# Kernel tuning notes

Measured on AMD Instinct MI355X. Metric: run time of the kernel, lower is better.

Reference implementation:

```python
import jax, jax.numpy as jnp
import numpy as np
from jax import lax

B, S, D, H = 2, 2048, 1024, 16
DH = D // H
KERNELS = (3, 5)
NK = len(KERNELS)
COUT = D // NK  # channels per conv branch


def setup_inputs() -> dict:
    key = jax.random.key(0)
    ks = jax.random.split(key, 12)
    w = lambda k, shp: (jax.random.normal(k, shp, dtype=jnp.float32) * 0.02)
    inp = {
        "q": jax.random.normal(ks[0], (B, S, D), dtype=jnp.float32),
        "k": jax.random.normal(ks[1], (B, S, D), dtype=jnp.float32),
        "v": jax.random.normal(ks[2], (B, S, D), dtype=jnp.float32),
        "mask": jnp.ones((B, S, S), dtype=jnp.int32),
        "Wq": w(ks[3], (D, D)),
        "Wk": w(ks[4], (D, D)),
        "Wv": w(ks[5], (D, D)),
        "Wo": w(ks[6], (D, D)),
        "bo": jnp.zeros((D,), dtype=jnp.float32),
        "conv_w0": w(ks[7], (COUT, D, KERNELS[0])),  # OIH
        "conv_b0": jnp.zeros((COUT,), dtype=jnp.float32),
        "conv_w1": w(ks[8], (COUT, D, KERNELS[1])),
        "conv_b1": jnp.zeros((COUT,), dtype=jnp.float32),
        "gate": jnp.ones((H,), dtype=jnp.float32),
    }
    return inp


def _split_heads(x):  # [B,S,D] -> [B,H,S,DH]
    return x.reshape(B, S, H, DH).transpose(0, 2, 1, 3)


def _conv1d_same(x_ncl, w_oik, b, ksz):
    pad = ksz // 2
    y = lax.conv_general_dilated(
        x_ncl, w_oik, window_strides=(1,), padding=[(pad, pad)],
        dimension_numbers=("NCH", "OIH", "NCH"))
    return y + b[None, :, None]


def reference(q, k, v, mask, Wq, Wk, Wv, Wo, bo,
              conv_w0, conv_b0, conv_w1, conv_b1, gate):
    qh = _split_heads(q @ Wq.T)
    kh = _split_heads(k @ Wk.T)
    vh = _split_heads(v @ Wv.T)

    # conv-derived K: operate on raw k in NCL layout, concat channel-wise
    k_ncl = k.transpose(0, 2, 1)  # [B,D,S]
    c0 = _conv1d_same(k_ncl, conv_w0, conv_b0, KERNELS[0])
    c1 = _conv1d_same(k_ncl, conv_w1, conv_b1, KERNELS[1])
    k_conv = jnp.concatenate([c0, c1], axis=1).transpose(0, 2, 1)  # [B,S,D]
    kch = _split_heads(k_conv)

    g = jax.nn.sigmoid(gate).reshape(1, H, 1, 1)
    scale = 1.0 / np.sqrt(DH).astype(np.float32)
    attn = ((1.0 - g) * jnp.einsum("bhqd,bhkd->bhqk", qh, kh)
            + g * jnp.einsum("bhqd,bhkd->bhqk", qh, kch)) * scale
    attn = jnp.where(mask[:, None, :, :] == 0, jnp.float32(-1e9), attn)
    attn = jax.nn.softmax(attn, axis=-1)

    out = jnp.einsum("bhqk,bhkd->bhqd", attn, vh)  # [B,H,S,DH]
    out = out.transpose(0, 2, 1, 3).reshape(B, S, D)
    return out @ Wo.T + bo
```

## Files before the change

### kernel.cpp

```cpp
#include <hip/hip_runtime.h>
#include <math.h>

#define Bb 2
#define Ss 2048
#define Dd 1024
#define Hh 16
#define SP 2052

typedef unsigned short u16;
typedef __bf16 bf16x8 __attribute__((ext_vector_type(8)));
typedef float f32x4 __attribute__((ext_vector_type(4)));
typedef unsigned short u16x8 __attribute__((ext_vector_type(8)));

__device__ __forceinline__ u16 f2bf(float f) {
    union { float f; unsigned int u; } c; c.f = f;
    unsigned int u = c.u + 0x7FFFu + ((c.u >> 16) & 1u);
    return (u16)(u >> 16);
}

__device__ __forceinline__ u16 f2bfn(float f) {
    __bf16 h = (__bf16)f;
    union { __bf16 h; u16 u; } c; c.h = h;
    return c.u;
}

__device__ __forceinline__ float bf2f(u16 h) {
    union { unsigned int u; float f; } c; c.u = ((unsigned int)h) << 16;
    return c.f;
}

__device__ __forceinline__ void gload16(const void* g, void* l) {
    __builtin_amdgcn_global_load_lds(
        (const __attribute__((address_space(1))) void*)g,
        (__attribute__((address_space(3))) void*)l, 16, 0, 0);
}

__global__ void prep_weights(const float* __restrict__ Wq, const float* __restrict__ Wk,
                             const float* __restrict__ Wv, const float* __restrict__ Wo,
                             const float* __restrict__ w0, const float* __restrict__ b0,
                             const float* __restrict__ w1, const float* __restrict__ b1,
                             const float* __restrict__ gate,
                             u16* __restrict__ wqs, u16* __restrict__ wvb, u16* __restrict__ wob,
                             u16* __restrict__ Wc0, u16* __restrict__ Wc1, float* __restrict__ bc)
{
    int idx = blockIdx.x * 256 + threadIdx.x;
    const int NW = 1024 * 1024;
    if (idx < NW) { wqs[idx] = f2bf(Wq[idx] * 0.18033688011112042f); return; }
    idx -= NW;
    if (idx < NW) { wvb[idx] = f2bf(Wv[idx]); return; }
    idx -= NW;
    if (idx < NW) { wob[idx] = f2bf(Wo[idx]); return; }
    idx -= NW;
    if (idx < 512 * 3072) {
        int c = idx / 3072, rem = idx % 3072, t = rem >> 10, d = rem & 1023;
        float g = 1.f / (1.f + expf(-gate[c >> 6]));
        float v = g * w0[(c * 1024 + d) * 3 + t];
        if (t == 1) v += (1.f - g) * Wk[c * 1024 + d];
        Wc0[idx] = f2bf(v);
        return;
    }
    idx -= 512 * 3072;
    if (idx < 512 * 5120) {
        int c = idx / 5120, rem = idx % 5120, t = rem >> 10, d = rem & 1023;
        int cg = c + 512;
        float g = 1.f / (1.f + expf(-gate[cg >> 6]));
        float v = g * w1[(c * 1024 + d) * 5 + t];
        if (t == 2) v += (1.f - g) * Wk[cg * 1024 + d];
        Wc1[idx] = f2bf(v);
        return;
    }
    idx -= 512 * 5120;
    if (idx < 1024) {
        float g = 1.f / (1.f + expf(-gate[idx >> 6]));
        bc[idx] = g * (idx < 512 ? b0[idx] : b1[idx - 512]);
    }
}

__global__ void convert_inputs(const float* __restrict__ q, const float* __restrict__ k,
                               const float* __restrict__ v,
                               u16* __restrict__ qbf, u16* __restrict__ kbf, u16* __restrict__ vbf)
{
    int idx = blockIdx.x * 256 + threadIdx.x;
    const int per = (Bb * SP * Dd) / 8;
    int which = idx / per;
    if (which >= 3) return;
    int e = (idx - which * per) * 8;
    const float* src = which == 0 ? q : which == 1 ? k : v;
    u16* dst = which == 0 ? qbf : which == 1 ? kbf : vbf;
    int rp = e >> 10, col = e & 1023;
    int b = rp / SP, r = rp - b * SP;
    u16x8 o;
    if (r >= 2 && r < SP - 2) {
        const float* s = &src[((size_t)b * Ss + (r - 2)) * Dd + col];
        float4 lo = *(const float4*)s, hi = *(const float4*)(s + 4);
        o[0] = f2bf(lo.x); o[1] = f2bf(lo.y); o[2] = f2bf(lo.z); o[3] = f2bf(lo.w);
        o[4] = f2bf(hi.x); o[5] = f2bf(hi.y); o[6] = f2bf(hi.z); o[7] = f2bf(hi.w);
    } else {
        #pragma unroll
        for (int j = 0; j < 8; j++) o[j] = 0;
    }
    *(u16x8*)&dst[e] = o;
}

__global__ void mask_prep(const int* __restrict__ mask, unsigned int* __restrict__ bits,
                          int* __restrict__ rowflags)
{
    int row = blockIdx.x;
    int lane = threadIdx.x;
    const int* mp = mask + (size_t)row * Ss + lane * 32;
    unsigned int w = 0;
    #pragma unroll
    for (int j = 0; j < 32; j += 4) {
        int4 m4 = *(const int4*)&mp[j];
        if (m4.x != 0) w |= 1u << j;
        if (m4.y != 0) w |= 1u << (j + 1);
        if (m4.z != 0) w |= 1u << (j + 2);
        if (m4.w != 0) w |= 1u << (j + 3);
    }
    bits[(size_t)row * 64 + lane] = w;
    int anyz = __any(w != 0xFFFFFFFFu);
    if (lane == 0) rowflags[row] = anyz;
}

__device__ __forceinline__ void run_gemm_job(
    const u16* __restrict__ A, const u16* __restrict__ B, u16* __restrict__ C,
    int strB, int kS, int kL, int mB, int nB, int rO, int Cst,
    u16* As, u16* Bsh, int lane, int wave, int waveM, int waveN)
{
    f32x4 acc[4][4];
    #pragma unroll
    for (int i = 0; i < 4; i++)
        #pragma unroll
        for (int j = 0; j < 4; j++) acc[i][j] = (f32x4){0.f, 0.f, 0.f, 0.f};

    for (int k0 = kS; k0 < kS + kL; k0 += 32) {
        __syncthreads();
        #pragma unroll
        for (int cc = 0; cc < 2; cc++) {
            int rbase = (wave * 2 + cc) * 16;
            int r = rbase + (lane >> 2);
            int gm = mB + r;
            int grow = (gm >> 11) * SP + (gm & 2047) + rO + (k0 >> 10);
            int csrc = (lane & 3) ^ (r & 3);
            gload16(A + (size_t)grow * 1024 + (k0 & 1023) + csrc * 8, &As[rbase * 32]);
            int gn = nB + r;
            gload16(B + (size_t)gn * strB + k0 + csrc * 8, &Bsh[rbase * 32]);
        }
        __syncthreads();

        bf16x8 af[4], bfr[4];
        #pragma unroll
        for (int t = 0; t < 4; t++) {
            int mrow = waveM + t * 16 + (lane & 15);
            af[t] = *(const bf16x8*)&As[mrow * 32 + (((lane >> 4) ^ (mrow & 3))) * 8];
            int nrow = waveN + t * 16 + (lane & 15);
            bfr[t] = *(const bf16x8*)&Bsh[nrow * 32 + (((lane >> 4) ^ (nrow & 3))) * 8];
        }
        #pragma unroll
        for (int mt = 0; mt < 4; mt++)
            #pragma unroll
            for (int nt = 0; nt < 4; nt++)
                acc[mt][nt] = __builtin_amdgcn_mfma_f32_16x16x32_bf16(
                    af[mt], bfr[nt], acc[mt][nt], 0, 0, 0);
    }

    #pragma unroll
    for (int mt = 0; mt < 4; mt++)
        #pragma unroll
        for (int nt = 0; nt < 4; nt++)
            #pragma unroll
            for (int r = 0; r < 4; r++) {
                int row = mB + waveM + mt * 16 + (lane >> 4) * 4 + r;
                int gcol = nB + waveN + nt * 16 + (lane & 15);
                C[(size_t)row * Cst + gcol] = f2bf(acc[mt][nt][r]);
            }
}

__global__ __launch_bounds__(256) void gemm_multi(
    const u16* __restrict__ qbf, const u16* __restrict__ kbf, const u16* __restrict__ vbf,
    const u16* __restrict__ wqs, const u16* __restrict__ wvb,
    const u16* __restrict__ Wc0, const u16* __restrict__ Wc1,
    u16* __restrict__ Qp, u16* __restrict__ Vp,
    u16* __restrict__ P0a, u16* __restrict__ P0b,
    u16* __restrict__ P1a, u16* __restrict__ P1b, u16* __restrict__ P1c)
{
    __shared__ u16 As[128 * 32];
    __shared__ u16 Bsh[128 * 32];
    int tid = threadIdx.x, lane = tid & 63, wave = tid >> 6;
    int waveM = (wave >> 1) * 64, waveN = (wave & 1) * 64;

    int bid = blockIdx.x;
    const u16 *A0, *B0; u16 *C0; int sB0, kS0, kL0, mB0, nB0, rO0, Cs0;
    const u16 *A1 = nullptr, *B1 = nullptr; u16 *C1 = nullptr;
    int sB1 = 0, kS1 = 0, kL1 = 0, mB1 = 0, nB1 = 0, rO1 = 0, Cs1 = 0;
    int njobs = 1;

    if (bid < 128) {
        int t = bid;
        A0 = kbf; B0 = Wc0; C0 = P0a; sB0 = 3072; kS0 = 0; kL0 = 2048;
        mB0 = (t >> 2) * 128; nB0 = (t & 3) * 128; rO0 = 1; Cs0 = 512;
    } else if (bid < 256) {
        int t = bid - 128;
        A0 = kbf; B0 = Wc1; C0 = P1a; sB0 = 5120; kS0 = 0; kL0 = 2048;
        mB0 = (t >> 2) * 128; nB0 = (t & 3) * 128; rO0 = 0; Cs0 = 512;
    } else if (bid < 384) {
        int t = bid - 256;
        A0 = kbf; B0 = Wc1; C0 = P1b; sB0 = 5120; kS0 = 2048; kL0 = 2048;
        mB0 = (t >> 2) * 128; nB0 = (t & 3) * 128; rO0 = 0; Cs0 = 512;
    } else if (bid < 512) {
        int t = bid - 384;
        A0 = kbf; B0 = Wc0; C0 = P0b; sB0 = 3072; kS0 = 2048; kL0 = 1024;
        mB0 = (t >> 2) * 128; nB0 = (t & 3) * 128; rO0 = 1; Cs0 = 512;
        A1 = kbf; B1 = Wc1; C1 = P1c; sB1 = 5120; kS1 = 4096; kL1 = 1024;
        mB1 = mB0; nB1 = nB0; rO1 = 0; Cs1 = 512;
        njobs = 2;
    } else {
        int i0 = (bid - 512) * 2, i1 = i0 + 1;
        if (i0 < 256) { A0 = qbf; B0 = wqs; C0 = Qp; }
        else { i0 -= 256; A0 = vbf; B0 = wvb; C0 = Vp; }
        sB0 = 1024; kS0 = 0; kL0 = 1024;
        mB0 = (i0 >> 3) * 128; nB0 = (i0 & 7) * 128; rO0 = 2; Cs0 = 1024;
        if (i1 < 256) { A1 = qbf; B1 = wqs; C1 = Qp; }
        else { i1 -= 256; A1 = vbf; B1 = wvb; C1 = Vp; }
        sB1 = 1024; kS1 = 0; kL1 = 1024;
        mB1 = (i1 >> 3) * 128; nB1 = (i1 & 7) * 128; rO1 = 2; Cs1 = 1024;
        njobs = 2;
    }

    run_gemm_job(A0, B0, C0, sB0, kS0, kL0, mB0, nB0, rO0, Cs0,
                 As, Bsh, lane, wave, waveM, waveN);
    if (njobs == 2)
        run_gemm_job(A1, B1, C1, sB1, kS1, kL1, mB1, nB1, rO1, Cs1,
                     As, Bsh, lane, wave, waveM, waveN);
}

__global__ __launch_bounds__(256) void conv_reduce(
    const u16* __restrict__ P0a, const u16* __restrict__ P0b,
    const u16* __restrict__ P1a, const u16* __restrict__ P1b, const u16* __restrict__ P1c,
    const float* __restrict__ bc, u16* __restrict__ Keff)
{
    int idx = blockIdx.x * 256 + threadIdx.x;
    int e = idx * 8;
    int r = e >> 9, c = e & 511;
    u16x8 a0 = *(const u16x8*)&P0a[e];
    u16x8 b0 = *(const u16x8*)&P0b[e];
    u16x8 a1 = *(const u16x8*)&P1a[e];
    u16x8 b1 = *(const u16x8*)&P1b[e];
    u16x8 c1 = *(const u16x8*)&P1c[e];
    float bias0[8], bias1[8];
    *(float4*)&bias0[0] = *(const float4*)&bc[c];
    *(float4*)&bias0[4] = *(const float4*)&bc[c + 4];
    *(float4*)&bias1[0] = *(const float4*)&bc[512 + c];
    *(float4*)&bias1[4] = *(const float4*)&bc[512 + c + 4];
    u16x8 o0, o1;
    #pragma unroll
    for (int j = 0; j < 8; j++) {
        o0[j] = f2bf(bf2f(a0[j]) + bf2f(b0[j]) + bias0[j]);
        o1[j] = f2bf(bf2f(a1[j]) + bf2f(b1[j]) + bf2f(c1[j]) + bias1[j]);
    }
    *(u16x8*)&Keff[(size_t)r * 1024 + c] = o0;
    *(u16x8*)&Keff[(size_t)r * 1024 + 512 + c] = o1;
}

__global__ __launch_bounds__(256) void gemm_out(
    const u16* __restrict__ A, const u16* __restrict__ Bw,
    float* __restrict__ Cf32, const float* __restrict__ bias)
{
    __shared__ u16 As[128 * 32];
    __shared__ u16 Bs[128 * 32];
    int tid = threadIdx.x, lane = tid & 63, wave = tid >> 6;
    int waveM = (wave >> 1) * 64, waveN = (wave & 1) * 64;
    int mBase = blockIdx.y * 128, nBase = blockIdx.x * 128;
    const int K = 1024;

    f32x4 acc[4][4];
    #pragma unroll
    for (int i = 0; i < 4; i++)
        #pragma unroll
        for (int j = 0; j < 4; j++) acc[i][j] = (f32x4){0.f, 0.f, 0.f, 0.f};

    for (int k0 = 0; k0 < K; k0 += 32) {
        __syncthreads();
        #pragma unroll
        for (int cc = 0; cc < 2; cc++) {
            int rbase = (wave * 2 + cc) * 16;
            int r = rbase + (lane >> 2);
            int gm = mBase + r;
            int grow = (gm >> 11) * SP + (gm & 2047) + 2;
            int csrc = (lane & 3) ^ (r & 3);
            gload16(A + (size_t)grow * 1024 + k0 + csrc * 8, &As[rbase * 32]);
            int gn = nBase + r;
            gload16(Bw + (size_t)gn * K + k0 + csrc * 8, &Bs[rbase * 32]);
        }
        __syncthreads();

        bf16x8 af[4], bfr[4];
        #pragma unroll
        for (int t = 0; t < 4; t++) {
            int mrow = waveM + t * 16 + (lane & 15);
            af[t] = *(const bf16x8*)&As[mrow * 32 + (((lane >> 4) ^ (mrow & 3))) * 8];
            int nrow = waveN + t * 16 + (lane & 15);
            bfr[t] = *(const bf16x8*)&Bs[nrow * 32 + (((lane >> 4) ^ (nrow & 3))) * 8];
        }
        #pragma unroll
        for (int mt = 0; mt < 4; mt++)
            #pragma unroll
            for (int nt = 0; nt < 4; nt++)
                acc[mt][nt] = __builtin_amdgcn_mfma_f32_16x16x32_bf16(
                    af[mt], bfr[nt], acc[mt][nt], 0, 0, 0);
    }

    #pragma unroll
    for (int mt = 0; mt < 4; mt++)
        #pragma unroll
        for (int nt = 0; nt < 4; nt++)
            #pragma unroll
            for (int r = 0; r < 4; r++) {
                int row = mBase + waveM + mt * 16 + (lane >> 4) * 4 + r;
                int gcol = nBase + waveN + nt * 16 + (lane & 15);
                Cf32[(size_t)row * 1024 + gcol] = acc[mt][nt][r] + bias[gcol];
            }
}

__global__ __launch_bounds__(256) void vtrans_kernel(const u16* __restrict__ Vp,
                                                     u16* __restrict__ Vt)
{
    __shared__ u16 t[64 * 64];
    int bid = blockIdx.x;
    int st = bid & 31, h = (bid >> 5) & 15, b = bid >> 9;
    int s0 = st * 64;
    int tid = threadIdx.x;
    #pragma unroll
    for (int w = 0; w < 2; w++) {
        int f = tid + w * 256;
        int row = f >> 3, c = f & 7;
        int p = c ^ (row & 7);
        u16x8 v = *(const u16x8*)&Vp[(size_t)(b * Ss + s0 + row) * Dd + h * 64 + c * 8];
        *(u16x8*)&t[row * 64 + p * 8] = v;
    }
    __syncthreads();
    #pragma unroll
    for (int w = 0; w < 2; w++) {
        int f = tid + w * 256;
        int d = f >> 3, s8 = (f & 7) * 8;
        u16x8 v;
        #pragma unroll
        for (int j = 0; j < 8; j++) {
            int s = s8 + j;
            v[j] = t[s * 64 + (((d >> 3) ^ (s & 7))) * 8 + (d & 7)];
        }
        *(u16x8*)&Vt[((size_t)(b * Hh + h) * 64 + d) * Ss + s0 + s8] = v;
    }
}

__global__ __launch_bounds__(256) void flash_kernel(
    const u16* __restrict__ Qp, const u16* __restrict__ Keff, const u16* __restrict__ Vt,
    const unsigned int* __restrict__ maskbits, const int* __restrict__ rowflags,
    u16* __restrict__ AO)
{
    __shared__ u16 Qs[128 * 64];
    __shared__ u16 Ks[64 * 64];
    __shared__ u16 Ps[4][32 * 64];
    int tid = threadIdx.x, lane = tid & 63, wave = tid >> 6;

    int bid = blockIdx.x;
    int xcd = bid & 7, slot = bid >> 3;
    int grp = xcd * 4 + (slot >> 4);
    int q0 = (slot & 15) * 128;
    int h = grp & 15, b = grp >> 4;

    #pragma unroll
    for (int cc = 0; cc < 4; cc++) {
        int rbase = (wave * 4 + cc) * 8;
        int r = rbase + (lane >> 3);
        int csrc = (lane & 7) ^ (r & 7);
        gload16(Qp + (size_t)(b * Ss + q0 + r) * Dd + h * 64 + csrc * 8, &Qs[rbase * 64]);
    }

    int anyz = 0;
    #pragma unroll
    for (int mt = 0; mt < 2; mt++)
        #pragma unroll
        for (int r = 0; r < 4; r++)
            anyz |= rowflags[b * Ss + q0 + wave * 32 + mt * 16 + (lane >> 4) * 4 + r];
    bool doMask = __any(anyz);

    float lrow[2][4];
    f32x4 oa[2][4];
    #pragma unroll
    for (int mt = 0; mt < 2; mt++) {
        #pragma unroll
        for (int r = 0; r < 4; r++) lrow[mt][r] = 0.f;
        #pragma unroll
        for (int nt = 0; nt < 4; nt++) oa[mt][nt] = (f32x4){0.f, 0.f, 0.f, 0.f};
    }

    __syncthreads();

    bf16x8 qa[2][2];
    #pragma unroll
    for (int mt = 0; mt < 2; mt++)
        #pragma unroll
        for (int ks = 0; ks < 2; ks++) {
            int mr = wave * 32 + mt * 16 + (lane & 15);
            int c = ks * 4 + (lane >> 4);
            qa[mt][ks] = *(const bf16x8*)&Qs[mr * 64 + (c ^ (mr & 7)) * 8];
        }

    const u16* vbase = Vt + (size_t)(b * Hh + h) * 64 * Ss;

    for (int k0 = 0; k0 < Ss; k0 += 64) {
        #pragma unroll
        for (int cc = 0; cc < 2; cc++) {
            int rbase = (wave * 2 + cc) * 8;
            int r = rbase + (lane >> 3);
            int csrc = (lane & 7) ^ (r & 7);
            gload16(Keff + (size_t)(b * Ss + k0 + r) * Dd + h * 64 + csrc * 8, &Ks[rbase * 64]);
        }
        __syncthreads();

        f32x4 sa[2][4];
        #pragma unroll
        for (int mt = 0; mt < 2; mt++)
            #pragma unroll
            for (int nt = 0; nt < 4; nt++) sa[mt][nt] = (f32x4){0.f, 0.f, 0.f, 0.f};
        bf16x8 kb[4][2];
        #pragma unroll
        for (int nt = 0; nt < 4; nt++)
            #pragma unroll
            for (int ks = 0; ks < 2; ks++) {
                int nr = nt * 16 + (lane & 15);
                int c = ks * 4 + (lane >> 4);
                kb[nt][ks] = *(const bf16x8*)&Ks[nr * 64 + (c ^ (nr & 7)) * 8];
            }
        #pragma unroll
        for (int mt = 0; mt < 2; mt++)
            #pragma unroll
            for (int nt = 0; nt < 4; nt++)
                #pragma unroll
                for (int ks = 0; ks < 2; ks++)
                    sa[mt][nt] = __builtin_amdgcn_mfma_f32_16x16x32_bf16(
                        qa[mt][ks], kb[nt][ks], sa[mt][nt], 0, 0, 0);

        bf16x8 vf[4][2];
        #pragma unroll
        for (int nt = 0; nt < 4; nt++)
            #pragma unroll
            for (int ks = 0; ks < 2; ks++) {
                int d = nt * 16 + (lane & 15);
                int kc = k0 + ks * 32 + (lane >> 4) * 8;
                vf[nt][ks] = *(const bf16x8*)&vbase[(size_t)d * Ss + kc];
            }

        if (doMask) {
            #pragma unroll
            for (int mt = 0; mt < 2; mt++)
                #pragma unroll
                for (int r = 0; r < 4; r++) {
                    int qrow = q0 + wave * 32 + mt * 16 + (lane >> 4) * 4 + r;
                    const unsigned int* mb = &maskbits[((size_t)b * Ss + qrow) * 64 + (k0 >> 5)];
                    unsigned int w0m = mb[0], w1m = mb[1];
                    #pragma unroll
                    for (int nt = 0; nt < 4; nt++) {
                        int col = nt * 16 + (lane & 15);
                        unsigned int w = (col & 32) ? w1m : w0m;
                        if (!((w >> (col & 31)) & 1u)) sa[mt][nt][r] = -1.442695e9f;
                    }
                }
        }

        #pragma unroll
        for (int mt = 0; mt < 2; mt++)
            #pragma unroll
            for (int r = 0; r < 4; r++) {
                float p0 = __builtin_amdgcn_exp2f(sa[mt][0][r]);
                float p1 = __builtin_amdgcn_exp2f(sa[mt][1][r]);
                float p2 = __builtin_amdgcn_exp2f(sa[mt][2][r]);
                float p3 = __builtin_amdgcn_exp2f(sa[mt][3][r]);
                sa[mt][0][r] = p0; sa[mt][1][r] = p1;
                sa[mt][2][r] = p2; sa[mt][3][r] = p3;
                lrow[mt][r] += (p0 + p1) + (p2 + p3);
            }

        u16* pw = Ps[wave];
        #pragma unroll
        for (int mt = 0; mt < 2; mt++)
            #pragma unroll
            for (int nt = 0; nt < 4; nt++)
                #pragma unroll
                for (int r = 0; r < 4; r++) {
                    int row = mt * 16 + (lane >> 4) * 4 + r;
                    int col = nt * 16 + (lane & 15);
                    pw[row * 64 + (((col >> 3) ^ (row & 7))) * 8 + (col & 7)] =
                        f2bfn(sa[mt][nt][r]);
                }

        bf16x8 pa[2][2];
        #pragma unroll
        for (int mt = 0; mt < 2; mt++)
            #pragma unroll
            for (int ks = 0; ks < 2; ks++) {
                int row = mt * 16 + (lane & 15);
                int c = ks * 4 + (lane >> 4);
                pa[mt][ks] = *(const bf16x8*)&pw[row * 64 + (c ^ (row & 7)) * 8];
            }
        #pragma unroll
        for (int mt = 0; mt < 2; mt++)
            #pragma unroll
            for (int nt = 0; nt < 4; nt++)
                #pragma unroll
                for (int ks = 0; ks < 2; ks++)
                    oa[mt][nt] = __builtin_amdgcn_mfma_f32_16x16x32_bf16(
                        pa[mt][ks], vf[nt][ks], oa[mt][nt], 0, 0, 0);

        __syncthreads();
    }

    #pragma unroll
    for (int mt = 0; mt < 2; mt++)
        #pragma unroll
        for (int r = 0; r < 4; r++) {
            float rs = lrow[mt][r];
            #pragma unroll
            for (int d = 1; d < 16; d <<= 1) rs += __shfl_xor(rs, d, 64);
            float inv = 1.f / rs;
            int qrow = q0 + wave * 32 + mt * 16 + (lane >> 4) * 4 + r;
            size_t rowbase = ((size_t)b * SP + 2 + qrow) * Dd + h * 64;
            #pragma unroll
            for (int nt = 0; nt < 4; nt++)
                AO[rowbase + nt * 16 + (lane & 15)] = f2bfn(oa[mt][nt][r] * inv);
        }
}

extern "C" void kernel_launch(void* const* d_in, const int* in_sizes, int n_in,
                              void* d_out, int out_size, void* d_ws, size_t ws_size,
                              hipStream_t stream)
{
    (void)in_sizes; (void)n_in; (void)out_size; (void)ws_size;
    const float* q    = (const float*)d_in[0];
    const float* k    = (const float*)d_in[1];
    const float* v    = (const float*)d_in[2];
    const int*   mask = (const int*)d_in[3];
    const float* Wq   = (const float*)d_in[4];
    const float* Wk   = (const float*)d_in[5];
    const float* Wv   = (const float*)d_in[6];
    const float* Wo   = (const float*)d_in[7];
    const float* bo   = (const float*)d_in[8];
    const float* w0   = (const float*)d_in[9];
    const float* b0   = (const float*)d_in[10];
    const float* w1   = (const float*)d_in[11];
    const float* b1   = (const float*)d_in[12];
    const float* gate = (const float*)d_in[13];
    float* out = (float*)d_out;

    char* p = (char*)d_ws;
    const size_t nPad = (size_t)Bb * SP * Dd;
    const size_t nBSD = (size_t)Bb * Ss * Dd;
    const size_t nHalf = (size_t)4096 * 512;
    u16* qbf  = (u16*)p;            p += nPad * 2;
    u16* kbf  = (u16*)p;            p += nPad * 2;
    u16* vbf  = (u16*)p;            p += nPad * 2;
    u16* Qp   = (u16*)p;            p += nBSD * 2;
    u16* Keff = (u16*)p;            p += nBSD * 2;
    u16* Vp   = (u16*)p;            p += nBSD * 2;
    u16* Vt   = (u16*)p;            p += nBSD * 2;
    u16* wqs  = (u16*)p;            p += (size_t)Dd * Dd * 2;
    u16* wvb  = (u16*)p;            p += (size_t)Dd * Dd * 2;
    u16* wob  = (u16*)p;            p += (size_t)Dd * Dd * 2;
    u16* Wc0  = (u16*)p;            p += (size_t)512 * 3072 * 2;
    u16* Wc1  = (u16*)p;            p += (size_t)512 * 5120 * 2;
    float* bc = (float*)p;          p += 1024 * 4;
    unsigned int* mbits = (unsigned int*)p; p += (size_t)Bb * Ss * 64 * 4;
    int* rflags = (int*)p;          p += (size_t)Bb * Ss * 4;
    u16* P1a = (u16*)p;             p += nHalf * 2;
    u16* P1b = (u16*)p;             p += nHalf * 2;
    u16* P1c = (u16*)p;             p += nHalf * 2;
    u16* P0a = Vt;
    u16* P0b = Vt + nHalf;
    u16* AO = vbf;

    {
        int total = 3 * 1024 * 1024 + 512 * 3072 + 512 * 5120 + 1024;
        hipLaunchKernelGGL(prep_weights, dim3((total + 255) / 256), dim3(256), 0, stream,
                           Wq, Wk, Wv, Wo, w0, b0, w1, b1, gate,
                           wqs, wvb, wob, Wc0, Wc1, bc);
    }
    {
        int total = 3 * (Bb * SP * Dd) / 8;
        hipLaunchKernelGGL(convert_inputs, dim3((total + 255) / 256), dim3(256), 0, stream,
                           q, k, v, qbf, kbf, vbf);
    }
    hipLaunchKernelGGL(mask_prep, dim3(Bb * Ss), dim3(64), 0, stream, mask, mbits, rflags);

    hipLaunchKernelGGL(gemm_multi, dim3(768), dim3(256), 0, stream,
                       qbf, kbf, vbf, wqs, wvb, Wc0, Wc1, Qp, Vp,
                       P0a, P0b, P1a, P1b, P1c);
    hipLaunchKernelGGL(conv_reduce, dim3(1024), dim3(256), 0, stream,
                       P0a, P0b, P1a, P1b, P1c, bc, Keff);
    hipLaunchKernelGGL(vtrans_kernel, dim3(Bb * Hh * (Ss / 64)), dim3(256), 0, stream, Vp, Vt);
    hipLaunchKernelGGL(flash_kernel, dim3(512), dim3(256), 0, stream,
                       Qp, Keff, Vt, mbits, rflags, AO);
    hipLaunchKernelGGL(gemm_out, dim3(8, 32), dim3(256), 0, stream,
                       AO, wob, out, bo);
}
```

Baseline: 362.5 us.

## Split flash attention KV range in two and merge partial outputs

```diff
diff --git a/kernel.cpp b/kernel.cpp
--- a/kernel.cpp
+++ b/kernel.cpp
@@ -356,7 +356,7 @@
 __global__ __launch_bounds__(256) void flash_kernel(
     const u16* __restrict__ Qp, const u16* __restrict__ Keff, const u16* __restrict__ Vt,
     const unsigned int* __restrict__ maskbits, const int* __restrict__ rowflags,
-    u16* __restrict__ AO)
+    float* __restrict__ Op, float* __restrict__ lp)
 {
     __shared__ u16 Qs[128 * 64];
     __shared__ u16 Ks[64 * 64];
@@ -365,9 +365,12 @@
 
     int bid = blockIdx.x;
     int xcd = bid & 7, slot = bid >> 3;
-    int grp = xcd * 4 + (slot >> 4);
-    int q0 = (slot & 15) * 128;
+    int grp = xcd * 4 + (slot >> 5);
+    int sub = slot & 31;
+    int q0 = (sub >> 1) * 128;
+    int half = sub & 1;
     int h = grp & 15, b = grp >> 4;
+    int kv0 = half * (Ss / 2);
 
     #pragma unroll
     for (int cc = 0; cc < 4; cc++) {
@@ -409,7 +412,7 @@
 
     const u16* vbase = Vt + (size_t)(b * Hh + h) * 64 * Ss;
 
-    for (int k0 = 0; k0 < Ss; k0 += 64) {
+    for (int k0 = kv0; k0 < kv0 + Ss / 2; k0 += 64) {
         #pragma unroll
         for (int cc = 0; cc < 2; cc++) {
             int rbase = (wave * 2 + cc) * 8;
@@ -523,13 +526,44 @@
             float rs = lrow[mt][r];
             #pragma unroll
             for (int d = 1; d < 16; d <<= 1) rs += __shfl_xor(rs, d, 64);
-            float inv = 1.f / rs;
             int qrow = q0 + wave * 32 + mt * 16 + (lane >> 4) * 4 + r;
-            size_t rowbase = ((size_t)b * SP + 2 + qrow) * Dd + h * 64;
+            size_t rowbase = ((size_t)(half * Bb + b) * Ss + qrow) * Dd + h * 64;
             #pragma unroll
             for (int nt = 0; nt < 4; nt++)
-                AO[rowbase + nt * 16 + (lane & 15)] = f2bfn(oa[mt][nt][r] * inv);
-        }
+                Op[rowbase + nt * 16 + (lane & 15)] = oa[mt][nt][r];
+            if ((lane & 15) == 0)
+                lp[((size_t)(half * Bb + b) * Ss + qrow) * Hh + h] = rs;
+        }
+}
+
+__global__ __launch_bounds__(256) void flash_merge(
+    const float* __restrict__ Op, const float* __restrict__ lp,
+    u16* __restrict__ AO)
+{
+    int idx = blockIdx.x * 256 + threadIdx.x;
+    size_t e = (size_t)idx * 8;
+    int col = (int)(e & 1023);
+    int qrow = (int)((e >> 10) & (Ss - 1));
+    int b = (int)(e >> 21);
+    int h = col >> 6;
+    const size_t halfO = (size_t)Bb * Ss * Dd;
+    const size_t halfL = (size_t)Bb * Ss * Hh;
+    float4 a0 = *(const float4*)&Op[e];
+    float4 a1 = *(const float4*)&Op[e + 4];
+    float4 c0 = *(const float4*)&Op[halfO + e];
+    float4 c1 = *(const float4*)&Op[halfO + e + 4];
+    size_t li = ((size_t)b * Ss + qrow) * Hh + h;
+    float inv = 1.f / (lp[li] + lp[halfL + li]);
+    u16x8 o;
+    o[0] = f2bfn((a0.x + c0.x) * inv);
+    o[1] = f2bfn((a0.y + c0.y) * inv);
+    o[2] = f2bfn((a0.z + c0.z) * inv);
+    o[3] = f2bfn((a0.w + c0.w) * inv);
+    o[4] = f2bfn((a1.x + c1.x) * inv);
+    o[5] = f2bfn((a1.y + c1.y) * inv);
+    o[6] = f2bfn((a1.z + c1.z) * inv);
+    o[7] = f2bfn((a1.w + c1.w) * inv);
+    *(u16x8*)&AO[((size_t)b * SP + 2 + qrow) * Dd + col] = o;
 }
 
 extern "C" void kernel_launch(void* const* d_in, const int* in_sizes, int n_in,
@@ -575,6 +609,8 @@
     u16* P1a = (u16*)p;             p += nHalf * 2;
     u16* P1b = (u16*)p;             p += nHalf * 2;
     u16* P1c = (u16*)p;             p += nHalf * 2;
+    float* Op = (float*)p;          p += (size_t)2 * nBSD * 4;
+    float* lp = (float*)p;          p += (size_t)2 * Bb * Ss * Hh * 4;
     u16* P0a = Vt;
     u16* P0b = Vt + nHalf;
     u16* AO = vbf;
@@ -598,8 +634,9 @@
     hipLaunchKernelGGL(conv_reduce, dim3(1024), dim3(256), 0, stream,
                        P0a, P0b, P1a, P1b, P1c, bc, Keff);
     hipLaunchKernelGGL(vtrans_kernel, dim3(Bb * Hh * (Ss / 64)), dim3(256), 0, stream, Vp, Vt);
-    hipLaunchKernelGGL(flash_kernel, dim3(512), dim3(256), 0, stream,
-                       Qp, Keff, Vt, mbits, rflags, AO);
+    hipLaunchKernelGGL(flash_kernel, dim3(1024), dim3(256), 0, stream,
+                       Qp, Keff, Vt, mbits, rflags, Op, lp);
+    hipLaunchKernelGGL(flash_merge, dim3(4096), dim3(256), 0, stream, Op, lp, AO);
     hipLaunchKernelGGL(gemm_out, dim3(8, 32), dim3(256), 0, stream,
                        AO, wob, out, bo);
 }
```

After: 377.5 us. 4.1% more time.

## Fuse prep kernels, merge conv-reduce with V transpose, widen flash K tile

Applied to the files above, without the earlier changes.

```diff
diff --git a/kernel.cpp b/kernel.cpp
--- a/kernel.cpp
+++ b/kernel.cpp
@@ -35,91 +35,98 @@
         (__attribute__((address_space(3))) void*)l, 16, 0, 0);
 }
 
-__global__ void prep_weights(const float* __restrict__ Wq, const float* __restrict__ Wk,
-                             const float* __restrict__ Wv, const float* __restrict__ Wo,
-                             const float* __restrict__ w0, const float* __restrict__ b0,
-                             const float* __restrict__ w1, const float* __restrict__ b1,
-                             const float* __restrict__ gate,
-                             u16* __restrict__ wqs, u16* __restrict__ wvb, u16* __restrict__ wob,
-                             u16* __restrict__ Wc0, u16* __restrict__ Wc1, float* __restrict__ bc)
+#define PREP_WB 28676
+#define PREP_IB 6156
+#define PREP_MB 1024
+
+__global__ __launch_bounds__(256) void prep_all(
+    const float* __restrict__ Wq, const float* __restrict__ Wk,
+    const float* __restrict__ Wv, const float* __restrict__ Wo,
+    const float* __restrict__ w0, const float* __restrict__ b0,
+    const float* __restrict__ w1, const float* __restrict__ b1,
+    const float* __restrict__ gate,
+    const float* __restrict__ q, const float* __restrict__ k, const float* __restrict__ v,
+    const int* __restrict__ mask,
+    u16* __restrict__ wqs, u16* __restrict__ wvb, u16* __restrict__ wob,
+    u16* __restrict__ Wc0, u16* __restrict__ Wc1, float* __restrict__ bc,
+    u16* __restrict__ qbf, u16* __restrict__ kbf, u16* __restrict__ vbf,
+    unsigned int* __restrict__ bits, int* __restrict__ rowflags)
 {
-    int idx = blockIdx.x * 256 + threadIdx.x;
-    const int NW = 1024 * 1024;
-    if (idx < NW) { wqs[idx] = f2bf(Wq[idx] * 0.18033688011112042f); return; }
-    idx -= NW;
-    if (idx < NW) { wvb[idx] = f2bf(Wv[idx]); return; }
-    idx -= NW;
-    if (idx < NW) { wob[idx] = f2bf(Wo[idx]); return; }
-    idx -= NW;
-    if (idx < 512 * 3072) {
-        int c = idx / 3072, rem = idx % 3072, t = rem >> 10, d = rem & 1023;
-        float g = 1.f / (1.f + expf(-gate[c >> 6]));
-        float v = g * w0[(c * 1024 + d) * 3 + t];
-        if (t == 1) v += (1.f - g) * Wk[c * 1024 + d];
-        Wc0[idx] = f2bf(v);
+    int bid = blockIdx.x, tid = threadIdx.x;
+    if (bid < PREP_WB) {
+        int idx = bid * 256 + tid;
+        const int NW = 1024 * 1024;
+        if (idx < NW) { wqs[idx] = f2bf(Wq[idx] * 0.18033688011112042f); return; }
+        idx -= NW;
+        if (idx < NW) { wvb[idx] = f2bf(Wv[idx]); return; }
+        idx -= NW;
+        if (idx < NW) { wob[idx] = f2bf(Wo[idx]); return; }
+        idx -= NW;
+        if (idx < 512 * 3072) {
+            int c = idx / 3072, rem = idx % 3072, t = rem >> 10, d = rem & 1023;
+            float g = 1.f / (1.f + expf(-gate[c >> 6]));
+            float vv = g * w0[(c * 1024 + d) * 3 + t];
+            if (t == 1) vv += (1.f - g) * Wk[c * 1024 + d];
+            Wc0[idx] = f2bf(vv);
+            return;
+        }
+        idx -= 512 * 3072;
+        if (idx < 512 * 5120) {
+            int c = idx / 5120, rem = idx % 5120, t = rem >> 10, d = rem & 1023;
+            int cg = c + 512;
+            float g = 1.f / (1.f + expf(-gate[cg >> 6]));
+            float vv = g * w1[(c * 1024 + d) * 5 + t];
+            if (t == 2) vv += (1.f - g) * Wk[cg * 1024 + d];
+            Wc1[idx] = f2bf(vv);
+            return;
+        }
+        idx -= 512 * 5120;
+        if (idx < 1024) {
+            float g = 1.f / (1.f + expf(-gate[idx >> 6]));
+            bc[idx] = g * (idx < 512 ? b0[idx] : b1[idx - 512]);
+        }
         return;
     }
-    idx -= 512 * 3072;
-    if (idx < 512 * 5120) {
-        int c = idx / 5120, rem = idx % 5120, t = rem >> 10, d = rem & 1023;
-        int cg = c + 512;
-        float g = 1.f / (1.f + expf(-gate[cg >> 6]));
-        float v = g * w1[(c * 1024 + d) * 5 + t];
-        if (t == 2) v += (1.f - g) * Wk[cg * 1024 + d];
-        Wc1[idx] = f2bf(v);
+    if (bid < PREP_WB + PREP_IB) {
+        int idx = (bid - PREP_WB) * 256 + tid;
+        const int per = (Bb * SP * Dd) / 8;
+        int which = idx / per;
+        if (which >= 3) return;
+        int e = (idx - which * per) * 8;
+        const float* src = which == 0 ? q : which == 1 ? k : v;
+        u16* dst = which == 0 ? qbf : which == 1 ? kbf : vbf;
+        int rp = e >> 10, col = e & 1023;
+        int b = rp / SP, r = rp - b * SP;
+        u16x8 o;
+        if (r >= 2 && r < SP - 2) {
+            const float* s = &src[((size_t)b * Ss + (r - 2)) * Dd + col];
+            float4 lo = *(const float4*)s, hi = *(const float4*)(s + 4);
+            o[0] = f2bf(lo.x); o[1] = f2bf(lo.y); o[2] = f2bf(lo.z); o[3] = f2bf(lo.w);
+            o[4] = f2bf(hi.x); o[5] = f2bf(hi.y); o[6] = f2bf(hi.z); o[7] = f2bf(hi.w);
+        } else {
+            #pragma unroll
+            for (int j = 0; j < 8; j++) o[j] = 0;
+        }
+        *(u16x8*)&dst[e] = o;
         return;
     }
-    idx -= 512 * 5120;
-    if (idx < 1024) {
-        float g = 1.f / (1.f + expf(-gate[idx >> 6]));
-        bc[idx] = g * (idx < 512 ? b0[idx] : b1[idx - 512]);
-    }
-}
-
-__global__ void convert_inputs(const float* __restrict__ q, const float* __restrict__ k,
-                               const float* __restrict__ v,
-                               u16* __restrict__ qbf, u16* __restrict__ kbf, u16* __restrict__ vbf)
-{
-    int idx = blockIdx.x * 256 + threadIdx.x;
-    const int per = (Bb * SP * Dd) / 8;
-    int which = idx / per;
-    if (which >= 3) return;
-    int e = (idx - which * per) * 8;
-    const float* src = which == 0 ? q : which == 1 ? k : v;
-    u16* dst = which == 0 ? qbf : which == 1 ? kbf : vbf;
-    int rp = e >> 10, col = e & 1023;
-    int b = rp / SP, r = rp - b * SP;
-    u16x8 o;
-    if (r >= 2 && r < SP - 2) {
-        const float* s = &src[((size_t)b * Ss + (r - 2)) * Dd + col];
-        float4 lo = *(const float4*)s, hi = *(const float4*)(s + 4);
-        o[0] = f2bf(lo.x); o[1] = f2bf(lo.y); o[2] = f2bf(lo.z); o[3] = f2bf(lo.w);
-        o[4] = f2bf(hi.x); o[5] = f2bf(hi.y); o[6] = f2bf(hi.z); o[7] = f2bf(hi.w);
-    } else {
-        #pragma unroll
-        for (int j = 0; j < 8; j++) o[j] = 0;
-    }
-    *(u16x8*)&dst[e] = o;
-}
-
-__global__ void mask_prep(const int* __restrict__ mask, unsigned int* __restrict__ bits,
-                          int* __restrict__ rowflags)
-{
-    int row = blockIdx.x;
-    int lane = threadIdx.x;
-    const int* mp = mask + (size_t)row * Ss + lane * 32;
-    unsigned int w = 0;
-    #pragma unroll
-    for (int j = 0; j < 32; j += 4) {
-        int4 m4 = *(const int4*)&mp[j];
-        if (m4.x != 0) w |= 1u << j;
-        if (m4.y != 0) w |= 1u << (j + 1);
-        if (m4.z != 0) w |= 1u << (j + 2);
-        if (m4.w != 0) w |= 1u << (j + 3);
-    }
-    bits[(size_t)row * 64 + lane] = w;
-    int anyz = __any(w != 0xFFFFFFFFu);
-    if (lane == 0) rowflags[row] = anyz;
+    {
+        int row = (bid - PREP_WB - PREP_IB) * 4 + (tid >> 6);
+        int lane = tid & 63;
+        const int* mp = mask + (size_t)row * Ss + lane * 32;
+        unsigned int w = 0;
+        #pragma unroll
+        for (int j = 0; j < 32; j += 4) {
+            int4 m4 = *(const int4*)&mp[j];
+            if (m4.x != 0) w |= 1u << j;
+            if (m4.y != 0) w |= 1u << (j + 1);
+            if (m4.z != 0) w |= 1u << (j + 2);
+            if (m4.w != 0) w |= 1u << (j + 3);
+        }
+        bits[(size_t)row * 64 + lane] = w;
+        int anyz = __any(w != 0xFFFFFFFFu);
+        if (lane == 0) rowflags[row] = anyz;
+    }
 }
 
 __device__ __forceinline__ void run_gemm_job(
@@ -234,32 +241,64 @@
                      As, Bsh, lane, wave, waveM, waveN);
 }
 
-__global__ __launch_bounds__(256) void conv_reduce(
+__global__ __launch_bounds__(256) void reduce_trans(
     const u16* __restrict__ P0a, const u16* __restrict__ P0b,
     const u16* __restrict__ P1a, const u16* __restrict__ P1b, const u16* __restrict__ P1c,
-    const float* __restrict__ bc, u16* __restrict__ Keff)
+    const float* __restrict__ bc, u16* __restrict__ Keff,
+    const u16* __restrict__ Vp, u16* __restrict__ Vt)
 {
-    int idx = blockIdx.x * 256 + threadIdx.x;
-    int e = idx * 8;
-    int r = e >> 9, c = e & 511;
-    u16x8 a0 = *(const u16x8*)&P0a[e];
-    u16x8 b0 = *(const u16x8*)&P0b[e];
-    u16x8 a1 = *(const u16x8*)&P1a[e];
-    u16x8 b1 = *(const u16x8*)&P1b[e];
-    u16x8 c1 = *(const u16x8*)&P1c[e];
-    float bias0[8], bias1[8];
-    *(float4*)&bias0[0] = *(const float4*)&bc[c];
-    *(float4*)&bias0[4] = *(const float4*)&bc[c + 4];
-    *(float4*)&bias1[0] = *(const float4*)&bc[512 + c];
-    *(float4*)&bias1[4] = *(const float4*)&bc[512 + c + 4];
-    u16x8 o0, o1;
-    #pragma unroll
-    for (int j = 0; j < 8; j++) {
-        o0[j] = f2bf(bf2f(a0[j]) + bf2f(b0[j]) + bias0[j]);
-        o1[j] = f2bf(bf2f(a1[j]) + bf2f(b1[j]) + bf2f(c1[j]) + bias1[j]);
-    }
-    *(u16x8*)&Keff[(size_t)r * 1024 + c] = o0;
-    *(u16x8*)&Keff[(size_t)r * 1024 + 512 + c] = o1;
+    __shared__ u16 t[64 * 64];
+    int bid = blockIdx.x, tid = threadIdx.x;
+    if (bid < 1024) {
+        int idx = bid * 256 + tid;
+        int e = idx * 8;
+        int r = e >> 9, c = e & 511;
+        u16x8 a0 = *(const u16x8*)&P0a[e];
+        u16x8 b0 = *(const u16x8*)&P0b[e];
+        u16x8 a1 = *(const u16x8*)&P1a[e];
+        u16x8 b1 = *(const u16x8*)&P1b[e];
+        u16x8 c1 = *(const u16x8*)&P1c[e];
+        float bias0[8], bias1[8];
+        *(float4*)&bias0[0] = *(const float4*)&bc[c];
+        *(float4*)&bias0[4] = *(const float4*)&bc[c + 4];
+        *(float4*)&bias1[0] = *(const float4*)&bc[512 + c];
+        *(float4*)&bias1[4] = *(const float4*)&bc[512 + c + 4];
+        u16x8 o0, o1;
+        #pragma unroll
+        for (int j = 0; j < 8; j++) {
+            o0[j] = f2bf(bf2f(a0[j]) + bf2f(b0[j]) + bias0[j]);
+            o1[j] = f2bf(bf2f(a1[j]) + bf2f(b1[j]) + bf2f(c1[j]) + bias1[j]);
+        }
+        *(u16x8*)&Keff[(size_t)r * 1024 + c] = o0;
+        *(u16x8*)&Keff[(size_t)r * 1024 + 512 + c] = o1;
+        return;
+    }
+    {
+        int vb = bid - 1024;
+        int st = vb & 31, h = (vb >> 5) & 15, b = vb >> 9;
+        int s0 = st * 64;
+        #pragma unroll
+        for (int w = 0; w < 2; w++) {
+            int f = tid + w * 256;
+            int row = f >> 3, c = f & 7;
+            int p = c ^ (row & 7);
+            u16x8 vv = *(const u16x8*)&Vp[(size_t)(b * Ss + s0 + row) * Dd + h * 64 + c * 8];
+            *(u16x8*)&t[row * 64 + p * 8] = vv;
+        }
+        __syncthreads();
+        #pragma unroll
+        for (int w = 0; w < 2; w++) {
+            int f = tid + w * 256;
+            int d = f >> 3, s8 = (f & 7) * 8;
+            u16x8 vv;
+            #pragma unroll
+            for (int j = 0; j < 8; j++) {
+                int s = s8 + j;
+                vv[j] = t[s * 64 + (((d >> 3) ^ (s & 7))) * 8 + (d & 7)];
+            }
+            *(u16x8*)&Vt[((size_t)(b * Hh + h) * 64 + d) * Ss + s0 + s8] = vv;
+        }
+    }
 }
 
 __global__ __launch_bounds__(256) void gemm_out(
@@ -322,44 +361,13 @@
             }
 }
 
-__global__ __launch_bounds__(256) void vtrans_kernel(const u16* __restrict__ Vp,
-                                                     u16* __restrict__ Vt)
-{
-    __shared__ u16 t[64 * 64];
-    int bid = blockIdx.x;
-    int st = bid & 31, h = (bid >> 5) & 15, b = bid >> 9;
-    int s0 = st * 64;
-    int tid = threadIdx.x;
-    #pragma unroll
-    for (int w = 0; w < 2; w++) {
-        int f = tid + w * 256;
-        int row = f >> 3, c = f & 7;
-        int p = c ^ (row & 7);
-        u16x8 v = *(const u16x8*)&Vp[(size_t)(b * Ss + s0 + row) * Dd + h * 64 + c * 8];
-        *(u16x8*)&t[row * 64 + p * 8] = v;
-    }
-    __syncthreads();
-    #pragma unroll
-    for (int w = 0; w < 2; w++) {
-        int f = tid + w * 256;
-        int d = f >> 3, s8 = (f & 7) * 8;
-        u16x8 v;
-        #pragma unroll
-        for (int j = 0; j < 8; j++) {
-            int s = s8 + j;
-            v[j] = t[s * 64 + (((d >> 3) ^ (s & 7))) * 8 + (d & 7)];
-        }
-        *(u16x8*)&Vt[((size_t)(b * Hh + h) * 64 + d) * Ss + s0 + s8] = v;
-    }
-}
-
 __global__ __launch_bounds__(256) void flash_kernel(
     const u16* __restrict__ Qp, const u16* __restrict__ Keff, const u16* __restrict__ Vt,
     const unsigned int* __restrict__ maskbits, const int* __restrict__ rowflags,
     u16* __restrict__ AO)
 {
     __shared__ u16 Qs[128 * 64];
-    __shared__ u16 Ks[64 * 64];
+    __shared__ u16 Ks[128 * 64];
     __shared__ u16 Ps[4][32 * 64];
     int tid = threadIdx.x, lane = tid & 63, wave = tid >> 6;
 
@@ -409,109 +417,115 @@
 
     const u16* vbase = Vt + (size_t)(b * Hh + h) * 64 * Ss;
 
-    for (int k0 = 0; k0 < Ss; k0 += 64) {
-        #pragma unroll
-        for (int cc = 0; cc < 2; cc++) {
-            int rbase = (wave * 2 + cc) * 8;
+    for (int k0 = 0; k0 < Ss; k0 += 128) {
+        #pragma unroll
+        for (int cc = 0; cc < 4; cc++) {
+            int rbase = (wave * 4 + cc) * 8;
             int r = rbase + (lane >> 3);
             int csrc = (lane & 7) ^ (r & 7);
             gload16(Keff + (size_t)(b * Ss + k0 + r) * Dd + h * 64 + csrc * 8, &Ks[rbase * 64]);
         }
         __syncthreads();
 
-        f32x4 sa[2][4];
-        #pragma unroll
-        for (int mt = 0; mt < 2; mt++)
-            #pragma unroll
-            for (int nt = 0; nt < 4; nt++) sa[mt][nt] = (f32x4){0.f, 0.f, 0.f, 0.f};
-        bf16x8 kb[4][2];
-        #pragma unroll
-        for (int nt = 0; nt < 4; nt++)
-            #pragma unroll
-            for (int ks = 0; ks < 2; ks++) {
-                int nr = nt * 16 + (lane & 15);
-                int c = ks * 4 + (lane >> 4);
-                kb[nt][ks] = *(const bf16x8*)&Ks[nr * 64 + (c ^ (nr & 7)) * 8];
+        #pragma unroll
+        for (int half = 0; half < 2; half++) {
+            const u16* kh = &Ks[half * 64 * 64];
+
+            bf16x8 vf[4][2];
+            #pragma unroll
+            for (int nt = 0; nt < 4; nt++)
+                #pragma unroll
+                for (int ks = 0; ks < 2; ks++) {
+                    int d = nt * 16 + (lane & 15);
+                    int kc = k0 + half * 64 + ks * 32 + (lane >> 4) * 8;
+                    vf[nt][ks] = *(const bf16x8*)&vbase[(size_t)d * Ss + kc];
+                }
+
+            f32x4 sa[2][4];
+            #pragma unroll
+            for (int mt = 0; mt < 2; mt++)
+                #pragma unroll
+                for (int nt = 0; nt < 4; nt++) sa[mt][nt] = (f32x4){0.f, 0.f, 0.f, 0.f};
+            bf16x8 kb[4][2];
+            #pragma unroll
+            for (int nt = 0; nt < 4; nt++)
+                #pragma unroll
+                for (int ks = 0; ks < 2; ks++) {
+                    int nr = nt * 16 + (lane & 15);
+                    int c = ks * 4 + (lane >> 4);
+                    kb[nt][ks] = *(const bf16x8*)&kh[nr * 64 + (c ^ (nr & 7)) * 8];
+                }
+            #pragma unroll
+            for (int mt = 0; mt < 2; mt++)
+                #pragma unroll
+                for (int nt = 0; nt < 4; nt++)
+                    #pragma unroll
+                    for (int ks = 0; ks < 2; ks++)
+                        sa[mt][nt] = __builtin_amdgcn_mfma_f32_16x16x32_bf16(
+                            qa[mt][ks], kb[nt][ks], sa[mt][nt], 0, 0, 0);
+
+            if (doMask) {
+                #pragma unroll
+                for (int mt = 0; mt < 2; mt++)
+                    #pragma unroll
+                    for (int r = 0; r < 4; r++) {
+                        int qrow = q0 + wave * 32 + mt * 16 + (lane >> 4) * 4 + r;
+                        const unsigned int* mb =
+                            &maskbits[((size_t)b * Ss + qrow) * 64 + (k0 >> 5) + half * 2];
+                        unsigned int w0m = mb[0], w1m = mb[1];
+                        #pragma unroll
+                        for (int nt = 0; nt < 4; nt++) {
+                            int col = nt * 16 + (lane & 15);
+                            unsigned int w = (col & 32) ? w1m : w0m;
+                            if (!((w >> (col & 31)) & 1u)) sa[mt][nt][r] = -1.442695e9f;
+                        }
+                    }
             }
-        #pragma unroll
-        for (int mt = 0; mt < 2; mt++)
-            #pragma unroll
-            for (int nt = 0; nt < 4; nt++)
-                #pragma unroll
-                for (int ks = 0; ks < 2; ks++)
-                    sa[mt][nt] = __builtin_amdgcn_mfma_f32_16x16x32_bf16(
-                        qa[mt][ks], kb[nt][ks], sa[mt][nt], 0, 0, 0);
-
-        bf16x8 vf[4][2];
-        #pragma unroll
-        for (int nt = 0; nt < 4; nt++)
-            #pragma unroll
-            for (int ks = 0; ks < 2; ks++) {
-                int d = nt * 16 + (lane & 15);
-                int kc = k0 + ks * 32 + (lane >> 4) * 8;
-                vf[nt][ks] = *(const bf16x8*)&vbase[(size_t)d * Ss + kc];
-            }
-
-        if (doMask) {
+
             #pragma unroll
             for (int mt = 0; mt < 2; mt++)
                 #pragma unroll
                 for (int r = 0; r < 4; r++) {
-                    int qrow = q0 + wave * 32 + mt * 16 + (lane >> 4) * 4 + r;
-                    const unsigned int* mb = &maskbits[((size_t)b * Ss + qrow) * 64 + (k0 >> 5)];
-                    unsigned int w0m = mb[0], w1m = mb[1];
+                    float p0 = __builtin_amdgcn_exp2f(sa[mt][0][r]);
+                    float p1 = __builtin_amdgcn_exp2f(sa[mt][1][r]);
+                    float p2 = __builtin_amdgcn_exp2f(sa[mt][2][r]);
+                    float p3 = __builtin_amdgcn_exp2f(sa[mt][3][r]);
+                    sa[mt][0][r] = p0; sa[mt][1][r] = p1;
+                    sa[mt][2][r] = p2; sa[mt][3][r] = p3;
+                    lrow[mt][r] += (p0 + p1) + (p2 + p3);
+                }
+
+            u16* pw = Ps[wave];
+            #pragma unroll
+            for (int mt = 0; mt < 2; mt++)
+                #pragma unroll
+                for (int nt = 0; nt < 4; nt++)
                     #pragma unroll
-                    for (int nt = 0; nt < 4; nt++) {
+                    for (int r = 0; r < 4; r++) {
+                        int row = mt * 16 + (lane >> 4) * 4 + r;
                         int col = nt * 16 + (lane & 15);
-                        unsigned int w = (col & 32) ? w1m : w0m;
-                        if (!((w >> (col & 31)) & 1u)) sa[mt][nt][r] = -1.442695e9f;
+                        pw[row * 64 + (((col >> 3) ^ (row & 7))) * 8 + (col & 7)] =
+                            f2bfn(sa[mt][nt][r]);
                     }
+
+            bf16x8 pa[2][2];
+            #pragma unroll
+            for (int mt = 0; mt < 2; mt++)
+                #pragma unroll
+                for (int ks = 0; ks < 2; ks++) {
+                    int row = mt * 16 + (lane & 15);
+                    int c = ks * 4 + (lane >> 4);
+                    pa[mt][ks] = *(const bf16x8*)&pw[row * 64 + (c ^ (row & 7)) * 8];
                 }
-        }
-
-        #pragma unroll
-        for (int mt = 0; mt < 2; mt++)
-            #pragma unroll
-            for (int r = 0; r < 4; r++) {
-                float p0 = __builtin_amdgcn_exp2f(sa[mt][0][r]);
-                float p1 = __builtin_amdgcn_exp2f(sa[mt][1][r]);
-                float p2 = __builtin_amdgcn_exp2f(sa[mt][2][r]);
-                float p3 = __builtin_amdgcn_exp2f(sa[mt][3][r]);
-                sa[mt][0][r] = p0; sa[mt][1][r] = p1;
-                sa[mt][2][r] = p2; sa[mt][3][r] = p3;
-                lrow[mt][r] += (p0 + p1) + (p2 + p3);
-            }
-
-        u16* pw = Ps[wave];
-        #pragma unroll
-        for (int mt = 0; mt < 2; mt++)
-            #pragma unroll
-            for (int nt = 0; nt < 4; nt++)
-                #pragma unroll
-                for (int r = 0; r < 4; r++) {
-                    int row = mt * 16 + (lane >> 4) * 4 + r;
-                    int col = nt * 16 + (lane & 15);
-                    pw[row * 64 + (((col >> 3) ^ (row & 7))) * 8 + (col & 7)] =
-                        f2bfn(sa[mt][nt][r]);
-                }
-
-        bf16x8 pa[2][2];
-        #pragma unroll
-        for (int mt = 0; mt < 2; mt++)
-            #pragma unroll
-            for (int ks = 0; ks < 2; ks++) {
-                int row = mt * 16 + (lane & 15);
-                int c = ks * 4 + (lane >> 4);
-                pa[mt][ks] = *(const bf16x8*)&pw[row * 64 + (c ^ (row & 7)) * 8];
-            }
-        #pragma unroll
-        for (int mt = 0; mt < 2; mt++)
-            #pragma unroll
-            for (int nt = 0; nt < 4; nt++)
-                #pragma unroll
-                for (int ks = 0; ks < 2; ks++)
-                    oa[mt][nt] = __builtin_amdgcn_mfma_f32_16x16x32_bf16(
-                        pa[mt][ks], vf[nt][ks], oa[mt][nt], 0, 0, 0);
+            #pragma unroll
+            for (int mt = 0; mt < 2; mt++)
+                #pragma unroll
+                for (int nt = 0; nt < 4; nt++)
+                    #pragma unroll
+                    for (int ks = 0; ks < 2; ks++)
+                        oa[mt][nt] = __builtin_amdgcn_mfma_f32_16x16x32_bf16(
+                            pa[mt][ks], vf[nt][ks], oa[mt][nt], 0, 0, 0);
+        }
 
         __syncthreads();
     }
@@ -575,31 +589,26 @@
     u16* P1a = (u16*)p;             p += nHalf * 2;
     u16* P1b = (u16*)p;             p += nHalf * 2;
     u16* P1c = (u16*)p;             p += nHalf * 2;
-    u16* P0a = Vt;
-    u16* P0b = Vt + nHalf;
+    u16* P0a = (u16*)p;             p += nHalf * 2;
+    u16* P0b = (u16*)p;             p += nHalf * 2;
     u16* AO = vbf;
 
-    {
-        int total = 3 * 1024 * 1024 + 512 * 3072 + 512 * 5120 + 1024;
-        hipLaunchKernelGGL(prep_weights, dim3((total + 255) / 256), dim3(256), 0, stream,
-                           Wq, Wk, Wv, Wo, w0, b0, w1, b1, gate,
-                           wqs, wvb, wob, Wc0, Wc1, bc);
-    }
-    {
-        int total = 3 * (Bb * SP * Dd) / 8;
-        hipLaunchKernelGGL(convert_inputs, dim3((total + 255) / 256), dim3(256), 0, stream,
-                           q, k, v, qbf, kbf, vbf);
-    }
-    hipLaunchKernelGGL(mask_prep, dim3(Bb * Ss), dim3(64), 0, stream, mask, mbits, rflags);
+    hipLaunchKernelGGL(prep_all, dim3(PREP_WB + PREP_IB + PREP_MB), dim3(256), 0, stream,
+                       Wq, Wk, Wv, Wo, w0, b0, w1, b1, gate,
+                       q, k, v, mask,
+                       wqs, wvb, wob, Wc0, Wc1, bc,
+                       qbf, kbf, vbf, mbits, rflags);
 
     hipLaunchKernelGGL(gemm_multi, dim3(768), dim3(256), 0, stream,
                        qbf, kbf, vbf, wqs, wvb, Wc0, Wc1, Qp, Vp,
                        P0a, P0b, P1a, P1b, P1c);
-    hipLaunchKernelGGL(conv_reduce, dim3(1024), dim3(256), 0, stream,
-                       P0a, P0b, P1a, P1b, P1c, bc, Keff);
-    hipLaunchKernelGGL(vtrans_kernel, dim3(Bb * Hh * (Ss / 64)), dim3(256), 0, stream, Vp, Vt);
+
+    hipLaunchKernelGGL(reduce_trans, dim3(2048), dim3(256), 0, stream,
+                       P0a, P0b, P1a, P1b, P1c, bc, Keff, Vp, Vt);
+
     hipLaunchKernelGGL(flash_kernel, dim3(512), dim3(256), 0, stream,
                        Qp, Keff, Vt, mbits, rflags, AO);
+
     hipLaunchKernelGGL(gemm_out, dim3(8, 32), dim3(256), 0, stream,
                        AO, wob, out, bo);
 }
```

New measurement: 381.0 us. 1.05x slower.
